# Optimization experiments

Hardware: AMD Instinct MI355X
Metric: run time of the kernel (lower is better)

The kernel has to match this reference:

```python
import jax, jax.numpy as jnp
import numpy as np

N_HEADS = 8
CHUNK = 512


def _mha(x, Wq, Wk, Wv, Wo, n_heads):
    # Standard no-bias multi-head self-attention; torch Linear => x @ W.T
    B, T, d = x.shape
    hd = d // n_heads
    q = (x @ Wq.T).reshape(B, T, n_heads, hd)
    k = (x @ Wk.T).reshape(B, T, n_heads, hd)
    v = (x @ Wv.T).reshape(B, T, n_heads, hd)
    scores = jnp.einsum('bqhd,bkhd->bhqk', q, k) / jnp.sqrt(jnp.asarray(hd, x.dtype))
    attn = jax.nn.softmax(scores, axis=-1)
    out = jnp.einsum('bhqk,bkhd->bqhd', attn, v).reshape(B, T, d)
    return out @ Wo.T


def _cross_chunk_attn(s, n_heads):
    # SDPA over chunk summaries with q=k=v=s (no projections inside)
    B, nc, d = s.shape
    hd = d // n_heads
    q = s.reshape(B, nc, n_heads, hd)
    scores = jnp.einsum('bqhd,bkhd->bhqk', q, q) / jnp.sqrt(jnp.asarray(hd, s.dtype))
    attn = jax.nn.softmax(scores, axis=-1)
    out = jnp.einsum('bhqk,bkhd->bqhd', attn, q).reshape(B, nc, d)
    return out


def setup_inputs() -> dict:
    key = jax.random.key(0)
    ks = jax.random.split(key, 6)
    B, T, d = 2, 16384, 512
    scale = 1.0 / np.sqrt(d)
    x = jax.random.normal(ks[0], (B, T, d), dtype=jnp.float32)
    Wq = jax.random.normal(ks[1], (d, d), dtype=jnp.float32) * scale
    Wk = jax.random.normal(ks[2], (d, d), dtype=jnp.float32) * scale
    Wv = jax.random.normal(ks[3], (d, d), dtype=jnp.float32) * scale
    Wo = jax.random.normal(ks[4], (d, d), dtype=jnp.float32) * scale
    Wg = jax.random.normal(ks[5], (d, d), dtype=jnp.float32) * scale
    return {'x': x, 'Wq': Wq, 'Wk': Wk, 'Wv': Wv, 'Wo': Wo, 'Wg': Wg}


def reference(x, Wq, Wk, Wv, Wo, Wg):
    B, T, d = x.shape
    pad = (CHUNK - T % CHUNK) % CHUNK
    if pad > 0:
        x = jnp.pad(x, ((0, 0), (0, pad), (0, 0)))
    T_padded = T + pad
    n_chunks = T_padded // CHUNK
    # 1) chunk: (B*n_chunks, CHUNK, d)
    chunked = x.reshape(B * n_chunks, CHUNK, d)
    # 2) local attention within each chunk
    local_out = _mha(chunked, Wq, Wk, Wv, Wo, N_HEADS)
    # 3) mean-pool summaries -> (B, n_chunks, d)
    summaries = local_out.mean(axis=1).reshape(B, n_chunks, d)
    # 4) global projection + cross-chunk SDPA
    global_ctx = _cross_chunk_attn(summaries @ Wg.T, N_HEADS)
    # 5) broadcast chunk context back to tokens
    enriched = local_out + global_ctx.reshape(B * n_chunks, 1, d)
    # 6) recombine and trim padding
    out = enriched.reshape(B, T_padded, d)
    if pad > 0:
        out = out[:, :T, :]
    return out
```

## Files before the change

### kernel.cpp

```cpp
#include <hip/hip_runtime.h>

typedef __attribute__((ext_vector_type(8))) short short8;
typedef __attribute__((ext_vector_type(4))) float f32x4;
typedef __attribute__((ext_vector_type(16))) float f32x16;

#define DEV static __device__ __forceinline__

DEV float bf2f(unsigned short u) {
  union { unsigned int u32; float f; } v; v.u32 = ((unsigned int)u) << 16; return v.f;
}
DEV unsigned short f2bf(float f) {
  union { float f; unsigned int u; } v; v.f = f;
  unsigned int r = v.u + 0x7fffu + ((v.u >> 16) & 1u);
  return (unsigned short)(r >> 16);
}
DEV unsigned cvtpk(float lo, float hi) {
  unsigned r;
  asm("v_cvt_pk_bf16_f32 %0, %1, %2" : "=v"(r) : "v"(lo), "v"(hi));
  return r;
}
DEV void plswap(unsigned &a, unsigned &b) {
  asm("v_permlane32_swap_b32 %0, %1" : "+v"(a), "+v"(b));
}
DEV short8 mk8(unsigned a, unsigned b, unsigned c, unsigned d) {
  union { unsigned u[4]; short8 v; } x;
  x.u[0] = a; x.u[1] = b; x.u[2] = c; x.u[3] = d; return x.v;
}
DEV float fexp2(float x) {
  float r;
  asm("v_exp_f32 %0, %1" : "=v"(r) : "v"(x));
  return r;
}

#define GLL16(g, l) __builtin_amdgcn_global_load_lds( \
    (const __attribute__((address_space(1))) void*)(g), \
    (__attribute__((address_space(3))) void*)(l), 16, 0, 0)

constexpr int D  = 512;
constexpr int BT = 32768;

__global__ __launch_bounds__(256) void k_convert(
    const float* __restrict__ x, const float* __restrict__ Wq, const float* __restrict__ Wk,
    const float* __restrict__ Wv, const float* __restrict__ Wo,
    unsigned short* __restrict__ xb, unsigned short* __restrict__ wqkv,
    unsigned short* __restrict__ wo_b) {
  int idx = blockIdx.x * 256 + threadIdx.x;
  const int NX4 = (BT * D) / 4;
  const float* src; unsigned short* dst; size_t i4;
  if (idx < NX4) {
    src = x; dst = xb; i4 = (size_t)idx * 4;
  } else {
    int t = idx - NX4;
    int w = t >> 16;
    int within = t & 65535;
    src = (w == 0) ? Wq : (w == 1) ? Wk : (w == 2) ? Wv : Wo;
    dst = (w < 3) ? (wqkv + (size_t)w * D * D) : wo_b;
    i4 = (size_t)within * 4;
  }
  float4 v = *(const float4*)(src + i4);
  ushort4 o; o.x = f2bf(v.x); o.y = f2bf(v.y); o.z = f2bf(v.z); o.w = f2bf(v.w);
  *(ushort4*)(dst + i4) = o;
}

template<int NBLK, int EPI>
__global__ __launch_bounds__(512, 4) void k_gemm(
    const unsigned short* __restrict__ A, const unsigned short* __restrict__ Bm,
    unsigned short* __restrict__ O0, unsigned short* __restrict__ O1,
    unsigned short* __restrict__ O2) {
  __shared__ unsigned short Ash[3][128 * 32];
  __shared__ unsigned short Bsh[3][256 * 32];
  const int tid = threadIdx.x;
  const int lane = tid & 63, w = tid >> 6;
  const int lr = lane & 15, lg = lane >> 4;
  const int cpx = gridDim.x >> 3;
  const int bid = blockIdx.x;
  const int work = (bid & 7) * cpx + (bid >> 3);
  const int nb = work % NBLK, mb = work / NBLK;
  const int m0 = mb * 128, n0 = nb * 256;
  const int wr = w >> 2, wc = w & 3;

  const int sr = lane >> 2;
  const int sg8 = ((lane & 3) ^ ((lane >> 3) & 3)) * 8;
  const unsigned short* gA  = A  + (size_t)(m0 + w * 16 + sr) * D + sg8;
  const unsigned short* gB0 = Bm + (size_t)(n0 + w * 16 + sr) * D + sg8;
  const unsigned short* gB1 = Bm + (size_t)(n0 + 128 + w * 16 + sr) * D + sg8;

  auto stage = [&](int kt, int b) {
    GLL16(gA  + kt * 32, &Ash[b][w * 512]);
    GLL16(gB0 + kt * 32, &Bsh[b][w * 512]);
    GLL16(gB1 + kt * 32, &Bsh[b][(128 + w * 16) * 32]);
  };

  f32x4 acc[4][4];
  #pragma unroll
  for (int m = 0; m < 4; ++m)
    #pragma unroll
    for (int n = 0; n < 4; ++n) acc[m][n] = (f32x4){0.f, 0.f, 0.f, 0.f};

  stage(0, 0);
  stage(1, 1);

  const int rdsw = (lg ^ ((lr >> 1) & 3)) * 8;

#define GSTEP(KT, WN) { \
    asm volatile("s_waitcnt vmcnt(" #WN ")" ::: "memory"); \
    __builtin_amdgcn_s_barrier(); \
    if ((KT) + 2 < 16) stage((KT) + 2, ((KT) + 2) % 3); \
    const unsigned short* Ac = Ash[(KT) % 3]; \
    const unsigned short* Bc = Bsh[(KT) % 3]; \
    short8 af[4], bf[4]; \
    _Pragma("unroll") \
    for (int m = 0; m < 4; ++m) \
      af[m] = *(const short8*)&Ac[(wr * 64 + m * 16 + lr) * 32 + rdsw]; \
    _Pragma("unroll") \
    for (int n = 0; n < 4; ++n) \
      bf[n] = *(const short8*)&Bc[(wc * 64 + n * 16 + lr) * 32 + rdsw]; \
    __builtin_amdgcn_s_setprio(1); \
    _Pragma("unroll") \
    for (int m = 0; m < 4; ++m) \
      _Pragma("unroll") \
      for (int n = 0; n < 4; ++n) \
        acc[m][n] = __builtin_amdgcn_mfma_f32_16x16x32_bf16(af[m], bf[n], acc[m][n], 0, 0, 0); \
    __builtin_amdgcn_s_setprio(0); \
  }

  GSTEP(0, 3)  GSTEP(1, 3)  GSTEP(2, 3)  GSTEP(3, 3)
  GSTEP(4, 3)  GSTEP(5, 3)  GSTEP(6, 3)  GSTEP(7, 3)
  GSTEP(8, 3)  GSTEP(9, 3)  GSTEP(10, 3) GSTEP(11, 3)
  GSTEP(12, 3) GSTEP(13, 3) GSTEP(14, 3) GSTEP(15, 0)
#undef GSTEP

  if (EPI == 1 && nb >= 4) {
    #pragma unroll
    for (int m = 0; m < 4; ++m) {
      #pragma unroll
      for (int n = 0; n < 4; ++n) {
        int e = (n0 - 1024) + wc * 64 + n * 16 + lr;
        int grow = m0 + wr * 64 + m * 16 + lg * 4;
        int bc = grow >> 9, key = grow & 511;
        ushort4 pk;
        pk.x = f2bf(acc[m][n][0]); pk.y = f2bf(acc[m][n][1]);
        pk.z = f2bf(acc[m][n][2]); pk.w = f2bf(acc[m][n][3]);
        *(ushort4*)&O2[(size_t)(bc * 512 + e) * 512 + key] = pk;
      }
    }
  } else {
    unsigned short* Od = O0;
    int cshift = 0;
    float cs = (EPI == 1 && nb < 2) ? 0.1803368801f : 1.0f;
    if (EPI == 1 && nb >= 2) { Od = O1; cshift = 512; }
    #pragma unroll
    for (int m = 0; m < 4; ++m) {
      #pragma unroll
      for (int n = 0; n < 4; ++n) {
        int col = n0 + wc * 64 + n * 16 + lr - cshift;
        #pragma unroll
        for (int r = 0; r < 4; ++r) {
          int row = m0 + wr * 64 + m * 16 + lg * 4 + r;
          Od[(size_t)row * D + col] = f2bf(acc[m][n][r] * cs);
        }
      }
    }
  }
}

__global__ __launch_bounds__(512, 4) void k_attn(
    const unsigned short* __restrict__ Q, const unsigned short* __restrict__ K,
    const unsigned short* __restrict__ Vt, unsigned short* __restrict__ attn_out) {
  __shared__ char lds[3][16384];
  const int tid = threadIdx.x;
  const int lane = tid & 63, w = tid >> 6;
  const int l31 = lane & 31, hl = lane >> 5;
  int work = ((blockIdx.x & 7) << 7) + (blockIdx.x >> 3);
  int qh = work & 1, h = (work >> 1) & 7, bc = work >> 4;
  int qbase = bc * 512 + qh * 256 + w * 32;

  short8 qf[4];
  {
    const unsigned short* qp = Q + (size_t)(qbase + l31) * D + h * 64 + hl * 8;
    #pragma unroll
    for (int ks = 0; ks < 4; ++ks) qf[ks] = *(const short8*)(qp + ks * 16);
  }

  const int lr3 = lane >> 3;
  const int srow = w * 8 + lr3;
  const int sq = (lane & 7) ^ ((lr3 + w) & 7);
  const unsigned short* gK = K  + (size_t)(bc * 512 + srow) * D + h * 64 + sq * 8;
  const unsigned short* gV = Vt + (size_t)(bc * 512 + h * 64 + srow) * D + sq * 8;
  auto STAGE = [&](int T, int B) {
    GLL16(gK + (size_t)(T) * 64 * D, &lds[B][w * 1024]);
    GLL16(gV + (T) * 64,             &lds[B][8192 + w * 1024]);
  };

  f32x16 oA, oB;
  #pragma unroll
  for (int i = 0; i < 16; ++i) { oA[i] = 0.f; oB[i] = 0.f; }
  float mrun = -3e38f, lrun = 0.f;
  const int f0 = (l31 + (l31 >> 3)) & 7;
  const int f1 = (f0 + 4) & 7;

  STAGE(0, 0);
  STAGE(1, 1);

  #pragma unroll
  for (int t = 0; t < 8; ++t) {
    if (t == 0 || t == 7) asm volatile("s_waitcnt vmcnt(0)" ::: "memory");
    else                  asm volatile("s_waitcnt vmcnt(2)" ::: "memory");
    __builtin_amdgcn_s_barrier();
    if (t < 6) STAGE(t + 2, (t + 2) % 3);
    const char* kb = lds[t % 3];
    const char* vb = lds[t % 3] + 8192;

    f32x16 sA, sB;
    #pragma unroll
    for (int i = 0; i < 16; ++i) { sA[i] = 0.f; sB[i] = 0.f; }
    #pragma unroll
    for (int ks = 0; ks < 4; ++ks) {
      int c = ks * 2 + hl;
      short8 kf0 = *(const short8*)(kb + l31 * 128 + ((c ^ f0) << 4));
      short8 kf1 = *(const short8*)(kb + (32 + l31) * 128 + ((c ^ f1) << 4));
      sA = __builtin_amdgcn_mfma_f32_32x32x16_bf16(kf0, qf[ks], sA, 0, 0, 0);
      sB = __builtin_amdgcn_mfma_f32_32x32x16_bf16(kf1, qf[ks], sB, 0, 0, 0);
    }

    float pm = fmaxf(sA[0], sA[1]);
    #pragma unroll
    for (int i = 2; i < 16; i += 2) pm = fmaxf(pm, fmaxf(sA[i], sA[i + 1]));
    #pragma unroll
    for (int i = 0; i < 16; i += 2) pm = fmaxf(pm, fmaxf(sB[i], sB[i + 1]));
    pm = fmaxf(pm, __shfl_xor(pm, 32));
    if (!__all(pm - mrun <= 8.f)) {
      float mnew = fmaxf(mrun, pm);
      float alpha = fexp2(mrun - mnew);
      mrun = mnew;
      lrun *= alpha;
      #pragma unroll
      for (int i = 0; i < 16; ++i) { oA[i] *= alpha; oB[i] *= alpha; }
    }
    float ls = 0.f;
    #pragma unroll
    for (int i = 0; i < 16; ++i) { float p = fexp2(sA[i] - mrun); sA[i] = p; ls += p; }
    #pragma unroll
    for (int i = 0; i < 16; ++i) { float p = fexp2(sB[i] - mrun); sB[i] = p; ls += p; }
    ls += __shfl_xor(ls, 32);
    lrun += ls;

    unsigned dA[8], dB[8];
    #pragma unroll
    for (int i = 0; i < 8; ++i) {
      dA[i] = cvtpk(sA[2 * i], sA[2 * i + 1]);
      dB[i] = cvtpk(sB[2 * i], sB[2 * i + 1]);
    }
    plswap(dA[0], dA[2]); plswap(dA[1], dA[3]);
    plswap(dA[4], dA[6]); plswap(dA[5], dA[7]);
    plswap(dB[0], dB[2]); plswap(dB[1], dB[3]);
    plswap(dB[4], dB[6]); plswap(dB[5], dB[7]);
    short8 pf[4] = { mk8(dA[0], dA[1], dA[2], dA[3]), mk8(dA[4], dA[5], dA[6], dA[7]),
                     mk8(dB[0], dB[1], dB[2], dB[3]), mk8(dB[4], dB[5], dB[6], dB[7]) };

    #pragma unroll
    for (int k4 = 0; k4 < 4; ++k4) {
      int c = k4 * 2 + hl;
      short8 vf0 = *(const short8*)(vb + l31 * 128 + ((c ^ f0) << 4));
      short8 vf1 = *(const short8*)(vb + (32 + l31) * 128 + ((c ^ f1) << 4));
      oA = __builtin_amdgcn_mfma_f32_32x32x16_bf16(vf0, pf[k4], oA, 0, 0, 0);
      oB = __builtin_amdgcn_mfma_f32_32x32x16_bf16(vf1, pf[k4], oB, 0, 0, 0);
    }
  }

  __syncthreads();
  float inv = 1.f / lrun;
  const int x7 = l31 & 7;
  char* tr = &lds[0][0] + w * 4096;
  #pragma unroll
  for (int r = 0; r < 16; ++r) {
    int e0 = (r & 3) + 8 * (r >> 2) + 4 * hl;
    *(unsigned short*)(tr + ((l31 * 128 + e0 * 2) ^ (x7 << 4)))        = f2bf(oA[r] * inv);
    *(unsigned short*)(tr + ((l31 * 128 + (32 + e0) * 2) ^ (x7 << 4))) = f2bf(oB[r] * inv);
  }
  unsigned short* op = attn_out + (size_t)(qbase + l31) * D + h * 64 + hl * 32;
  #pragma unroll
  for (int s = 0; s < 4; ++s) {
    int slot = (hl * 4 + s) ^ x7;
    short8 v = *(const short8*)(tr + l31 * 128 + slot * 16);
    *(short8*)(op + s * 8) = v;
  }
}

__global__ __launch_bounds__(256) void k_mean(const unsigned short* __restrict__ lout,
                                              float* __restrict__ summ) {
  int bc = blockIdx.x;
  int col = blockIdx.y * 256 + threadIdx.x;
  const unsigned short* p = lout + (size_t)bc * 512 * 512 + col;
  float s = 0.f;
  #pragma unroll 8
  for (int r = 0; r < 512; ++r) s += bf2f(p[(size_t)r * 512]);
  summ[bc * 512 + col] = s * (1.f / 512.f);
}

__global__ __launch_bounds__(256) void k_sg(const float* __restrict__ summ,
                                            const float* __restrict__ Wg,
                                            float* __restrict__ sg) {
  __shared__ float srow[512];
  int m = blockIdx.x >> 1, half = blockIdx.x & 1;
  for (int i = threadIdx.x; i < 512; i += 256) srow[i] = summ[m * 512 + i];
  __syncthreads();
  int n = half * 256 + threadIdx.x;
  const float* wr = Wg + (size_t)n * 512;
  float s = 0.f;
  #pragma unroll 8
  for (int kk = 0; kk < 512; ++kk) s += srow[kk] * wr[kk];
  sg[m * 512 + n] = s;
}

__global__ __launch_bounds__(256) void k_gattn(const float* __restrict__ sg,
                                               float* __restrict__ gctx) {
  __shared__ float qs[32][64];
  __shared__ float sc[32][32];
  int b = blockIdx.x >> 3, h = blockIdx.x & 7;
  int tid = threadIdx.x;
  for (int i = tid; i < 2048; i += 256) {
    int r = i >> 6, e = i & 63;
    qs[r][e] = sg[(size_t)(b * 32 + r) * 512 + h * 64 + e];
  }
  __syncthreads();
  for (int p = tid; p < 1024; p += 256) {
    int qi = p >> 5, ki = p & 31;
    float s = 0.f;
    #pragma unroll 8
    for (int e = 0; e < 64; ++e) s += qs[qi][e] * qs[ki][e];
    sc[qi][ki] = s * 0.125f;
  }
  __syncthreads();
  if (tid < 32) {
    float mx = -1e30f;
    for (int k2 = 0; k2 < 32; ++k2) mx = fmaxf(mx, sc[tid][k2]);
    float sm = 0.f;
    for (int k2 = 0; k2 < 32; ++k2) { float p = __expf(sc[tid][k2] - mx); sc[tid][k2] = p; sm += p; }
    float iv = 1.f / sm;
    for (int k2 = 0; k2 < 32; ++k2) sc[tid][k2] *= iv;
  }
  __syncthreads();
  for (int i = tid; i < 2048; i += 256) {
    int r = i >> 6, e = i & 63;
    float o = 0.f;
    #pragma unroll 8
    for (int k2 = 0; k2 < 32; ++k2) o += sc[r][k2] * qs[k2][e];
    gctx[(size_t)(b * 32 + r) * 512 + h * 64 + e] = o;
  }
}

__global__ __launch_bounds__(256) void k_final(const unsigned short* __restrict__ lout,
                                               const float* __restrict__ gctx,
                                               float* __restrict__ out) {
  size_t idx = (size_t)blockIdx.x * 256 + threadIdx.x;
  size_t i = idx * 4;
  int c = (int)(i & 511);
  int bcg = (int)(i >> 18);
  ushort4 lv = *(const ushort4*)(lout + i);
  float4 g = *(const float4*)(gctx + (size_t)bcg * 512 + c);
  float4 o;
  o.x = bf2f(lv.x) + g.x;
  o.y = bf2f(lv.y) + g.y;
  o.z = bf2f(lv.z) + g.z;
  o.w = bf2f(lv.w) + g.w;
  *(float4*)(out + i) = o;
}

extern "C" void kernel_launch(void* const* d_in, const int* in_sizes, int n_in,
                              void* d_out, int out_size, void* d_ws, size_t ws_size,
                              hipStream_t stream) {
  const float* x  = (const float*)d_in[0];
  const float* Wq = (const float*)d_in[1];
  const float* Wk = (const float*)d_in[2];
  const float* Wv = (const float*)d_in[3];
  const float* Wo = (const float*)d_in[4];
  const float* Wg = (const float*)d_in[5];
  float* out = (float*)d_out;

  char* ws = (char*)d_ws;
  unsigned short* xb   = (unsigned short*)(ws);
  unsigned short* q    = (unsigned short*)(ws + 33554432);
  unsigned short* kb   = (unsigned short*)(ws + 67108864);
  unsigned short* vt   = (unsigned short*)(ws + 100663296);
  unsigned short* wqkv = (unsigned short*)(ws + 134217728);
  unsigned short* wo_b = (unsigned short*)(ws + 135790592);
  float* summ = (float*)(ws + 136314880);
  float* sgp  = (float*)(ws + 136445952);
  float* gctx = (float*)(ws + 136577024);
  unsigned short* attn_out = xb;
  unsigned short* local_bf = q;

  k_convert<<<17408, 256, 0, stream>>>(x, Wq, Wk, Wv, Wo, xb, wqkv, wo_b);
  k_gemm<6, 1><<<1536, 512, 0, stream>>>(xb, wqkv, q, kb, vt);
  k_attn<<<1024, 512, 0, stream>>>(q, kb, vt, attn_out);
  k_gemm<2, 0><<<512, 512, 0, stream>>>(attn_out, wo_b, local_bf, nullptr, nullptr);
  k_mean<<<dim3(64, 2), 256, 0, stream>>>(local_bf, summ);
  k_sg<<<128, 256, 0, stream>>>(summ, Wg, sgp);
  k_gattn<<<16, 256, 0, stream>>>(sgp, gctx);
  k_final<<<16384, 256, 0, stream>>>(local_bf, gctx, out);
}
```

Baseline: 232.3 us.

## Enlarge GEMM tiles to 256x256 with 64-wide K double-buffered pipeline

The GEMM kernel moves from 128x256 tiles with a 3-stage, 32-wide K ring to 256x256 tiles with double-buffered 64-wide K steps split into two half-phases. Each wave now holds 8x4 accumulators and reuses its B fragments across two M halves. This raises arithmetic intensity and halves the number of blocks and barriers per unit of work. The cost is lower occupancy (launch bounds 2), higher register pressure, a 128KB LDS footprint and no read swizzle, so LDS bank conflicts are possible.

```diff
diff --git a/kernel.cpp b/kernel.cpp
--- a/kernel.cpp
+++ b/kernel.cpp
@@ -63,84 +63,94 @@
 }
 
 template<int NBLK, int EPI>
-__global__ __launch_bounds__(512, 4) void k_gemm(
+__global__ __launch_bounds__(512, 2) void k_gemm(
     const unsigned short* __restrict__ A, const unsigned short* __restrict__ Bm,
     unsigned short* __restrict__ O0, unsigned short* __restrict__ O1,
     unsigned short* __restrict__ O2) {
-  __shared__ unsigned short Ash[3][128 * 32];
-  __shared__ unsigned short Bsh[3][256 * 32];
+  __shared__ unsigned short sh[65536];
   const int tid = threadIdx.x;
   const int lane = tid & 63, w = tid >> 6;
   const int lr = lane & 15, lg = lane >> 4;
   const int cpx = gridDim.x >> 3;
-  const int bid = blockIdx.x;
-  const int work = (bid & 7) * cpx + (bid >> 3);
+  const int work = (blockIdx.x & 7) * cpx + (blockIdx.x >> 3);
   const int nb = work % NBLK, mb = work / NBLK;
-  const int m0 = mb * 128, n0 = nb * 256;
+  const int m0 = mb * 256, n0 = nb * 256;
   const int wr = w >> 2, wc = w & 3;
 
-  const int sr = lane >> 2;
-  const int sg8 = ((lane & 3) ^ ((lane >> 3) & 3)) * 8;
-  const unsigned short* gA  = A  + (size_t)(m0 + w * 16 + sr) * D + sg8;
-  const unsigned short* gB0 = Bm + (size_t)(n0 + w * 16 + sr) * D + sg8;
-  const unsigned short* gB1 = Bm + (size_t)(n0 + 128 + w * 16 + sr) * D + sg8;
-
-  auto stage = [&](int kt, int b) {
-    GLL16(gA  + kt * 32, &Ash[b][w * 512]);
-    GLL16(gB0 + kt * 32, &Bsh[b][w * 512]);
-    GLL16(gB1 + kt * 32, &Bsh[b][(128 + w * 16) * 32]);
-  };
-
-  f32x4 acc[4][4];
-  #pragma unroll
-  for (int m = 0; m < 4; ++m)
+  const int srow = tid >> 2;
+  const int scol = (tid & 3) * 8;
+  const unsigned short* gA = A  + (size_t)(m0 + srow) * D + scol;
+  const unsigned short* gB = Bm + (size_t)(n0 + srow) * D + scol;
+
+  f32x4 acc[8][4];
+  #pragma unroll
+  for (int m = 0; m < 8; ++m)
     #pragma unroll
     for (int n = 0; n < 4; ++n) acc[m][n] = (f32x4){0.f, 0.f, 0.f, 0.f};
 
-  stage(0, 0);
-  stage(1, 1);
-
-  const int rdsw = (lg ^ ((lr >> 1) & 3)) * 8;
-
-#define GSTEP(KT, WN) { \
-    asm volatile("s_waitcnt vmcnt(" #WN ")" ::: "memory"); \
-    __builtin_amdgcn_s_barrier(); \
-    if ((KT) + 2 < 16) stage((KT) + 2, ((KT) + 2) % 3); \
-    const unsigned short* Ac = Ash[(KT) % 3]; \
-    const unsigned short* Bc = Bsh[(KT) % 3]; \
-    short8 af[4], bf[4]; \
+  GLL16(gA,                 &sh[w * 512]);
+  GLL16(gA + 128 * D,       &sh[4096 + w * 512]);
+  GLL16(gB,                 &sh[32768 + w * 512]);
+  GLL16(gB + 128 * D,       &sh[32768 + 4096 + w * 512]);
+  GLL16(gA + 32,            &sh[8192 + w * 512]);
+  GLL16(gA + 128 * D + 32,  &sh[8192 + 4096 + w * 512]);
+  GLL16(gB + 32,            &sh[32768 + 8192 + w * 512]);
+  GLL16(gB + 128 * D + 32,  &sh[32768 + 8192 + 4096 + w * 512]);
+
+  short8 bfr[4];
+
+#define PHASE(T, MH, KS, SM, SKS) { \
+    if ((T) < 7) { \
+      const unsigned short* g = (SM) ? gB : gA; \
+      const int sb = ((SM) ? 32768 : 0) + ((((T) & 1) ^ 1) * 2 + (SKS)) * 8192; \
+      GLL16(g + ((T) + 1) * 64 + (SKS) * 32,           &sh[sb + w * 512]); \
+      GLL16(g + 128 * D + ((T) + 1) * 64 + (SKS) * 32, &sh[sb + 4096 + w * 512]); \
+    } \
+    const int aB = (((T) & 1) * 2 + (KS)) * 8192; \
+    const int bB = 32768 + (((T) & 1) * 2 + (KS)) * 8192; \
+    if ((MH) == 0) { \
+      _Pragma("unroll") \
+      for (int n = 0; n < 4; ++n) \
+        bfr[n] = *(const short8*)&sh[bB + (wc * 64 + n * 16 + lr) * 32 + lg * 8]; \
+    } \
+    short8 afr[4]; \
     _Pragma("unroll") \
-    for (int m = 0; m < 4; ++m) \
-      af[m] = *(const short8*)&Ac[(wr * 64 + m * 16 + lr) * 32 + rdsw]; \
-    _Pragma("unroll") \
-    for (int n = 0; n < 4; ++n) \
-      bf[n] = *(const short8*)&Bc[(wc * 64 + n * 16 + lr) * 32 + rdsw]; \
+    for (int mf = 0; mf < 4; ++mf) \
+      afr[mf] = *(const short8*)&sh[aB + (wr * 128 + (MH) * 64 + mf * 16 + lr) * 32 + lg * 8]; \
     __builtin_amdgcn_s_setprio(1); \
     _Pragma("unroll") \
-    for (int m = 0; m < 4; ++m) \
+    for (int mf = 0; mf < 4; ++mf) \
       _Pragma("unroll") \
       for (int n = 0; n < 4; ++n) \
-        acc[m][n] = __builtin_amdgcn_mfma_f32_16x16x32_bf16(af[m], bf[n], acc[m][n], 0, 0, 0); \
+        acc[(MH) * 4 + mf][n] = __builtin_amdgcn_mfma_f32_16x16x32_bf16(afr[mf], bfr[n], acc[(MH) * 4 + mf][n], 0, 0, 0); \
     __builtin_amdgcn_s_setprio(0); \
   }
 
-  GSTEP(0, 3)  GSTEP(1, 3)  GSTEP(2, 3)  GSTEP(3, 3)
-  GSTEP(4, 3)  GSTEP(5, 3)  GSTEP(6, 3)  GSTEP(7, 3)
-  GSTEP(8, 3)  GSTEP(9, 3)  GSTEP(10, 3) GSTEP(11, 3)
-  GSTEP(12, 3) GSTEP(13, 3) GSTEP(14, 3) GSTEP(15, 0)
-#undef GSTEP
+  #pragma unroll
+  for (int t = 0; t < 8; ++t) {
+    asm volatile("s_waitcnt vmcnt(4)" ::: "memory");
+    __builtin_amdgcn_s_barrier();
+    PHASE(t, 0, 0, 0, 0)
+    PHASE(t, 1, 0, 1, 0)
+    if (t < 7) asm volatile("s_waitcnt vmcnt(4)" ::: "memory");
+    else       asm volatile("s_waitcnt vmcnt(0)" ::: "memory");
+    __builtin_amdgcn_s_barrier();
+    PHASE(t, 0, 1, 0, 1)
+    PHASE(t, 1, 1, 1, 1)
+  }
+#undef PHASE
 
   if (EPI == 1 && nb >= 4) {
     #pragma unroll
-    for (int m = 0; m < 4; ++m) {
+    for (int mf = 0; mf < 8; ++mf) {
       #pragma unroll
       for (int n = 0; n < 4; ++n) {
         int e = (n0 - 1024) + wc * 64 + n * 16 + lr;
-        int grow = m0 + wr * 64 + m * 16 + lg * 4;
+        int grow = m0 + wr * 128 + mf * 16 + lg * 4;
         int bc = grow >> 9, key = grow & 511;
         ushort4 pk;
-        pk.x = f2bf(acc[m][n][0]); pk.y = f2bf(acc[m][n][1]);
-        pk.z = f2bf(acc[m][n][2]); pk.w = f2bf(acc[m][n][3]);
+        pk.x = f2bf(acc[mf][n][0]); pk.y = f2bf(acc[mf][n][1]);
+        pk.z = f2bf(acc[mf][n][2]); pk.w = f2bf(acc[mf][n][3]);
         *(ushort4*)&O2[(size_t)(bc * 512 + e) * 512 + key] = pk;
       }
     }
@@ -150,14 +160,14 @@
     float cs = (EPI == 1 && nb < 2) ? 0.1803368801f : 1.0f;
     if (EPI == 1 && nb >= 2) { Od = O1; cshift = 512; }
     #pragma unroll
-    for (int m = 0; m < 4; ++m) {
+    for (int mf = 0; mf < 8; ++mf) {
       #pragma unroll
       for (int n = 0; n < 4; ++n) {
         int col = n0 + wc * 64 + n * 16 + lr - cshift;
         #pragma unroll
         for (int r = 0; r < 4; ++r) {
-          int row = m0 + wr * 64 + m * 16 + lg * 4 + r;
-          Od[(size_t)row * D + col] = f2bf(acc[m][n][r] * cs);
+          int row = m0 + wr * 128 + mf * 16 + lg * 4 + r;
+          Od[(size_t)row * D + col] = f2bf(acc[mf][n][r] * cs);
         }
       }
     }
@@ -392,9 +402,9 @@
   unsigned short* local_bf = q;
 
   k_convert<<<17408, 256, 0, stream>>>(x, Wq, Wk, Wv, Wo, xb, wqkv, wo_b);
-  k_gemm<6, 1><<<1536, 512, 0, stream>>>(xb, wqkv, q, kb, vt);
+  k_gemm<6, 1><<<768, 512, 0, stream>>>(xb, wqkv, q, kb, vt);
   k_attn<<<1024, 512, 0, stream>>>(q, kb, vt, attn_out);
-  k_gemm<2, 0><<<512, 512, 0, stream>>>(attn_out, wo_b, local_bf, nullptr, nullptr);
+  k_gemm<2, 0><<<256, 512, 0, stream>>>(attn_out, wo_b, local_bf, nullptr, nullptr);
   k_mean<<<dim3(64, 2), 256, 0, stream>>>(local_bf, summ);
   k_sg<<<128, 256, 0, stream>>>(summ, Wg, sgp);
   k_gattn<<<16, 256, 0, stream>>>(sgp, gctx);
```

Result: no change. 230.4 us (-0.8%).

## Fuse fp32-to-bf16 conversion of x into the QKV projection GEMM

Applied to the files above, without the earlier changes.

The standalone pass that converted the full activation tensor x to bf16 now only converts the weights. The QKV GEMM loads fp32 x through registers, packs it to bf16 with v_cvt_pk_bf16_f32, and writes it into the LDS A tile one stage ahead, while B still uses direct global-to-LDS loads. This removes a full write and re-read of a bf16 copy of x. In exchange, the GEMM reads twice the bytes for A and adds register pressure and an extra LDS wait per k-step.

```diff
diff --git a/kernel.cpp b/kernel.cpp
--- a/kernel.cpp
+++ b/kernel.cpp
@@ -40,31 +40,22 @@
 constexpr int BT = 32768;
 
 __global__ __launch_bounds__(256) void k_convert(
-    const float* __restrict__ x, const float* __restrict__ Wq, const float* __restrict__ Wk,
+    const float* __restrict__ Wq, const float* __restrict__ Wk,
     const float* __restrict__ Wv, const float* __restrict__ Wo,
-    unsigned short* __restrict__ xb, unsigned short* __restrict__ wqkv,
-    unsigned short* __restrict__ wo_b) {
+    unsigned short* __restrict__ wqkv, unsigned short* __restrict__ wo_b) {
   int idx = blockIdx.x * 256 + threadIdx.x;
-  const int NX4 = (BT * D) / 4;
-  const float* src; unsigned short* dst; size_t i4;
-  if (idx < NX4) {
-    src = x; dst = xb; i4 = (size_t)idx * 4;
-  } else {
-    int t = idx - NX4;
-    int w = t >> 16;
-    int within = t & 65535;
-    src = (w == 0) ? Wq : (w == 1) ? Wk : (w == 2) ? Wv : Wo;
-    dst = (w < 3) ? (wqkv + (size_t)w * D * D) : wo_b;
-    i4 = (size_t)within * 4;
-  }
+  int w = idx >> 16;
+  int within = idx & 65535;
+  const float* src = (w == 0) ? Wq : (w == 1) ? Wk : (w == 2) ? Wv : Wo;
+  unsigned short* dst = (w < 3) ? (wqkv + (size_t)w * D * D) : wo_b;
+  size_t i4 = (size_t)within * 4;
   float4 v = *(const float4*)(src + i4);
   ushort4 o; o.x = f2bf(v.x); o.y = f2bf(v.y); o.z = f2bf(v.z); o.w = f2bf(v.w);
   *(ushort4*)(dst + i4) = o;
 }
 
-template<int NBLK, int EPI>
-__global__ __launch_bounds__(512, 4) void k_gemm(
-    const unsigned short* __restrict__ A, const unsigned short* __restrict__ Bm,
+__global__ __launch_bounds__(512, 4) void k_qkvf(
+    const float* __restrict__ Xf, const unsigned short* __restrict__ Bm,
     unsigned short* __restrict__ O0, unsigned short* __restrict__ O1,
     unsigned short* __restrict__ O2) {
   __shared__ unsigned short Ash[3][128 * 32];
@@ -75,18 +66,17 @@
   const int cpx = gridDim.x >> 3;
   const int bid = blockIdx.x;
   const int work = (bid & 7) * cpx + (bid >> 3);
-  const int nb = work % NBLK, mb = work / NBLK;
+  const int nb = work % 6, mb = work / 6;
   const int m0 = mb * 128, n0 = nb * 256;
   const int wr = w >> 2, wc = w & 3;
 
   const int sr = lane >> 2;
   const int sg8 = ((lane & 3) ^ ((lane >> 3) & 3)) * 8;
-  const unsigned short* gA  = A  + (size_t)(m0 + w * 16 + sr) * D + sg8;
+  const float* gAf = Xf + (size_t)(m0 + w * 16 + sr) * D + sg8;
   const unsigned short* gB0 = Bm + (size_t)(n0 + w * 16 + sr) * D + sg8;
   const unsigned short* gB1 = Bm + (size_t)(n0 + 128 + w * 16 + sr) * D + sg8;
 
-  auto stage = [&](int kt, int b) {
-    GLL16(gA  + kt * 32, &Ash[b][w * 512]);
+  auto stageB = [&](int kt, int b) {
     GLL16(gB0 + kt * 32, &Bsh[b][w * 512]);
     GLL16(gB1 + kt * 32, &Bsh[b][(128 + w * 16) * 32]);
   };
@@ -97,15 +87,35 @@
     #pragma unroll
     for (int n = 0; n < 4; ++n) acc[m][n] = (f32x4){0.f, 0.f, 0.f, 0.f};
 
-  stage(0, 0);
-  stage(1, 1);
+  float4 a0a, a0b, a1a, a1b;
+  { const float* p = gAf;      a0a = *(const float4*)p; a0b = *(const float4*)(p + 4); }
+  stageB(0, 0);
+  { const float* p = gAf + 32; a1a = *(const float4*)p; a1b = *(const float4*)(p + 4); }
+  stageB(1, 1);
+  {
+    short8 v = mk8(cvtpk(a0a.x, a0a.y), cvtpk(a0a.z, a0a.w),
+                   cvtpk(a0b.x, a0b.y), cvtpk(a0b.z, a0b.w));
+    *(short8*)((char*)&Ash[0][w * 512] + (size_t)lane * 16) = v;
+  }
+  asm volatile("s_waitcnt lgkmcnt(0)" ::: "memory");
+  __builtin_amdgcn_s_barrier();
 
   const int rdsw = (lg ^ ((lr >> 1) & 3)) * 8;
 
-#define GSTEP(KT, WN) { \
+#define QSTEP(KT, WN, SWA, SWB, SLA, SLB) { \
     asm volatile("s_waitcnt vmcnt(" #WN ")" ::: "memory"); \
+    if ((KT) < 15) { \
+      short8 v = mk8(cvtpk(SWA.x, SWA.y), cvtpk(SWA.z, SWA.w), \
+                     cvtpk(SWB.x, SWB.y), cvtpk(SWB.z, SWB.w)); \
+      *(short8*)((char*)&Ash[((KT) + 1) % 3][w * 512] + (size_t)lane * 16) = v; \
+      asm volatile("s_waitcnt lgkmcnt(0)" ::: "memory"); \
+    } \
     __builtin_amdgcn_s_barrier(); \
-    if ((KT) + 2 < 16) stage((KT) + 2, ((KT) + 2) % 3); \
+    if ((KT) + 2 < 16) { \
+      const float* p = gAf + ((KT) + 2) * 32; \
+      SLA = *(const float4*)p; SLB = *(const float4*)(p + 4); \
+      stageB((KT) + 2, ((KT) + 2) % 3); \
+    } \
     const unsigned short* Ac = Ash[(KT) % 3]; \
     const unsigned short* Bc = Bsh[(KT) % 3]; \
     short8 af[4], bf[4]; \
@@ -124,13 +134,17 @@
     __builtin_amdgcn_s_setprio(0); \
   }
 
-  GSTEP(0, 3)  GSTEP(1, 3)  GSTEP(2, 3)  GSTEP(3, 3)
-  GSTEP(4, 3)  GSTEP(5, 3)  GSTEP(6, 3)  GSTEP(7, 3)
-  GSTEP(8, 3)  GSTEP(9, 3)  GSTEP(10, 3) GSTEP(11, 3)
-  GSTEP(12, 3) GSTEP(13, 3) GSTEP(14, 3) GSTEP(15, 0)
-#undef GSTEP
-
-  if (EPI == 1 && nb >= 4) {
+  QSTEP(0, 2, a1a, a1b, a0a, a0b)   QSTEP(1, 2, a0a, a0b, a1a, a1b)
+  QSTEP(2, 2, a1a, a1b, a0a, a0b)   QSTEP(3, 2, a0a, a0b, a1a, a1b)
+  QSTEP(4, 2, a1a, a1b, a0a, a0b)   QSTEP(5, 2, a0a, a0b, a1a, a1b)
+  QSTEP(6, 2, a1a, a1b, a0a, a0b)   QSTEP(7, 2, a0a, a0b, a1a, a1b)
+  QSTEP(8, 2, a1a, a1b, a0a, a0b)   QSTEP(9, 2, a0a, a0b, a1a, a1b)
+  QSTEP(10, 2, a1a, a1b, a0a, a0b)  QSTEP(11, 2, a0a, a0b, a1a, a1b)
+  QSTEP(12, 2, a1a, a1b, a0a, a0b)  QSTEP(13, 2, a0a, a0b, a1a, a1b)
+  QSTEP(14, 2, a1a, a1b, a0a, a0b)  QSTEP(15, 0, a0a, a0b, a1a, a1b)
+#undef QSTEP
+
+  if (nb >= 4) {
     #pragma unroll
     for (int m = 0; m < 4; ++m) {
       #pragma unroll
@@ -147,8 +161,8 @@
   } else {
     unsigned short* Od = O0;
     int cshift = 0;
-    float cs = (EPI == 1 && nb < 2) ? 0.1803368801f : 1.0f;
-    if (EPI == 1 && nb >= 2) { Od = O1; cshift = 512; }
+    float cs = (nb < 2) ? 0.1803368801f : 1.0f;
+    if (nb >= 2) { Od = O1; cshift = 512; }
     #pragma unroll
     for (int m = 0; m < 4; ++m) {
       #pragma unroll
@@ -159,6 +173,86 @@
           int row = m0 + wr * 64 + m * 16 + lg * 4 + r;
           Od[(size_t)row * D + col] = f2bf(acc[m][n][r] * cs);
         }
+      }
+    }
+  }
+}
+
+__global__ __launch_bounds__(512, 4) void k_gemm(
+    const unsigned short* __restrict__ A, const unsigned short* __restrict__ Bm,
+    unsigned short* __restrict__ O0) {
+  __shared__ unsigned short Ash[3][128 * 32];
+  __shared__ unsigned short Bsh[3][256 * 32];
+  const int tid = threadIdx.x;
+  const int lane = tid & 63, w = tid >> 6;
+  const int lr = lane & 15, lg = lane >> 4;
+  const int cpx = gridDim.x >> 3;
+  const int bid = blockIdx.x;
+  const int work = (bid & 7) * cpx + (bid >> 3);
+  const int nb = work % 2, mb = work / 2;
+  const int m0 = mb * 128, n0 = nb * 256;
+  const int wr = w >> 2, wc = w & 3;
+
+  const int sr = lane >> 2;
+  const int sg8 = ((lane & 3) ^ ((lane >> 3) & 3)) * 8;
+  const unsigned short* gA  = A  + (size_t)(m0 + w * 16 + sr) * D + sg8;
+  const unsigned short* gB0 = Bm + (size_t)(n0 + w * 16 + sr) * D + sg8;
+  const unsigned short* gB1 = Bm + (size_t)(n0 + 128 + w * 16 + sr) * D + sg8;
+
+  auto stage = [&](int kt, int b) {
+    GLL16(gA  + kt * 32, &Ash[b][w * 512]);
+    GLL16(gB0 + kt * 32, &Bsh[b][w * 512]);
+    GLL16(gB1 + kt * 32, &Bsh[b][(128 + w * 16) * 32]);
+  };
+
+  f32x4 acc[4][4];
+  #pragma unroll
+  for (int m = 0; m < 4; ++m)
+    #pragma unroll
+    for (int n = 0; n < 4; ++n) acc[m][n] = (f32x4){0.f, 0.f, 0.f, 0.f};
+
+  stage(0, 0);
+  stage(1, 1);
+
+  const int rdsw = (lg ^ ((lr >> 1) & 3)) * 8;
+
+#define GSTEP(KT, WN) { \
+    asm volatile("s_waitcnt vmcnt(" #WN ")" ::: "memory"); \
+    __builtin_amdgcn_s_barrier(); \
+    if ((KT) + 2 < 16) stage((KT) + 2, ((KT) + 2) % 3); \
+    const unsigned short* Ac = Ash[(KT) % 3]; \
+    const unsigned short* Bc = Bsh[(KT) % 3]; \
+    short8 af[4], bf[4]; \
+    _Pragma("unroll") \
+    for (int m = 0; m < 4; ++m) \
+      af[m] = *(const short8*)&Ac[(wr * 64 + m * 16 + lr) * 32 + rdsw]; \
+    _Pragma("unroll") \
+    for (int n = 0; n < 4; ++n) \
+      bf[n] = *(const short8*)&Bc[(wc * 64 + n * 16 + lr) * 32 + rdsw]; \
+    __builtin_amdgcn_s_setprio(1); \
+    _Pragma("unroll") \
+    for (int m = 0; m < 4; ++m) \
+      _Pragma("unroll") \
+      for (int n = 0; n < 4; ++n) \
+        acc[m][n] = __builtin_amdgcn_mfma_f32_16x16x32_bf16(af[m], bf[n], acc[m][n], 0, 0, 0); \
+    __builtin_amdgcn_s_setprio(0); \
+  }
+
+  GSTEP(0, 3)  GSTEP(1, 3)  GSTEP(2, 3)  GSTEP(3, 3)
+  GSTEP(4, 3)  GSTEP(5, 3)  GSTEP(6, 3)  GSTEP(7, 3)
+  GSTEP(8, 3)  GSTEP(9, 3)  GSTEP(10, 3) GSTEP(11, 3)
+  GSTEP(12, 3) GSTEP(13, 3) GSTEP(14, 3) GSTEP(15, 0)
+#undef GSTEP
+
+  #pragma unroll
+  for (int m = 0; m < 4; ++m) {
+    #pragma unroll
+    for (int n = 0; n < 4; ++n) {
+      int col = n0 + wc * 64 + n * 16 + lr;
+      #pragma unroll
+      for (int r = 0; r < 4; ++r) {
+        int row = m0 + wr * 64 + m * 16 + lg * 4 + r;
+        O0[(size_t)row * D + col] = f2bf(acc[m][n][r]);
       }
     }
   }
@@ -379,7 +473,7 @@
   float* out = (float*)d_out;
 
   char* ws = (char*)d_ws;
-  unsigned short* xb   = (unsigned short*)(ws);
+  unsigned short* attn_out = (unsigned short*)(ws);
   unsigned short* q    = (unsigned short*)(ws + 33554432);
   unsigned short* kb   = (unsigned short*)(ws + 67108864);
   unsigned short* vt   = (unsigned short*)(ws + 100663296);
@@ -388,13 +482,12 @@
   float* summ = (float*)(ws + 136314880);
   float* sgp  = (float*)(ws + 136445952);
   float* gctx = (float*)(ws + 136577024);
-  unsigned short* attn_out = xb;
   unsigned short* local_bf = q;
 
-  k_convert<<<17408, 256, 0, stream>>>(x, Wq, Wk, Wv, Wo, xb, wqkv, wo_b);
-  k_gemm<6, 1><<<1536, 512, 0, stream>>>(xb, wqkv, q, kb, vt);
+  k_convert<<<1024, 256, 0, stream>>>(Wq, Wk, Wv, Wo, wqkv, wo_b);
+  k_qkvf<<<1536, 512, 0, stream>>>(x, wqkv, q, kb, vt);
   k_attn<<<1024, 512, 0, stream>>>(q, kb, vt, attn_out);
-  k_gemm<2, 0><<<512, 512, 0, stream>>>(attn_out, wo_b, local_bf, nullptr, nullptr);
+  k_gemm<<<512, 512, 0, stream>>>(attn_out, wo_b, local_bf);
   k_mean<<<dim3(64, 2), 256, 0, stream>>>(local_bf, summ);
   k_sg<<<128, 256, 0, stream>>>(summ, Wg, sgp);
   k_gattn<<<16, 256, 0, stream>>>(sgp, gctx);
```

Measured after the change: 239.5 us. +3.1%, slower.
